# Optimization experiments

Hardware: AMD Instinct MI355X
Metric: run time of the kernel (lower is better)

## Reference

```python
import jax, jax.numpy as jnp
import numpy as np
from jax import lax

DROP_PROB = 0.1
BLOCK_SIZE = 7
FEAT_SIZE = 56
GAMMA = DROP_PROB / BLOCK_SIZE ** 2 * (FEAT_SIZE ** 2 / (FEAT_SIZE - BLOCK_SIZE + 1) ** 2)


def setup_inputs() -> dict:
    key = jax.random.key(0)
    k1, k2 = jax.random.split(key)
    x = jax.random.normal(k1, (32, 256, 56, 56), dtype=jnp.float32)
    u = jax.random.uniform(k2, (56, 56), dtype=jnp.float32)
    return {"x": x, "u": u}


def reference(x, u):
    # Bernoulli(gamma) seed mask over (H, W)
    mask = (u < GAMMA).astype(x.dtype)
    # Original code scatters 1s at seed + offsets in [0, block)^2 (down/right),
    # then crops to (H, W). Equivalent: backward-looking max window of size block.
    dilated = lax.reduce_window(
        mask, jnp.array(0.0, x.dtype), lax.max,
        window_dimensions=(BLOCK_SIZE, BLOCK_SIZE),
        window_strides=(1, 1),
        padding=((BLOCK_SIZE - 1, 0), (BLOCK_SIZE - 1, 0)),
    )
    block_mask = 1.0 - dilated  # (H, W), 0 inside dropped blocks
    scale = block_mask.size / jnp.sum(block_mask)
    return x * block_mask[None, None, :, :] * scale
```

## Files before the change

### kernel.cpp

```cpp
#include <hip/hip_runtime.h>


#define HW      3136
#define WDIM    56
#define HDIM    56
#define HW4     784
#define ROWMASK 0x00FFFFFFFFFFFFFFull
#define NBLOCKS 2009u
#define STRIDE  514304u
#define NVEC    6422528u
#define REM     250880u

typedef float vfloat4 __attribute__((ext_vector_type(4)));

__global__ void __launch_bounds__(256, 8) dropblock_fused_kernel(
        const float* __restrict__ u, const vfloat4* __restrict__ x,
        vfloat4* __restrict__ out) {
    __shared__ unsigned long long chunks[49];
    __shared__ unsigned long long dropbits[HDIM];
    __shared__ float s_scale;

    const float gamma = (float)(0.1 / 49.0 * (3136.0 / 2500.0));

    const unsigned int t = blockIdx.x * 256u + threadIdx.x;
    const int lane = threadIdx.x & 63;
    const int wave = threadIdx.x >> 6;

    float u0  = u[threadIdx.x];
    float u1  = u[threadIdx.x + 256];
    float u2  = u[threadIdx.x + 512];
    float u3  = u[threadIdx.x + 768];
    float u4  = u[threadIdx.x + 1024];
    float u5  = u[threadIdx.x + 1280];
    float u6  = u[threadIdx.x + 1536];
    float u7  = u[threadIdx.x + 1792];
    float u8  = u[threadIdx.x + 2048];
    float u9  = u[threadIdx.x + 2304];
    float u10 = u[threadIdx.x + 2560];
    float u11 = u[threadIdx.x + 2816];
    float ulast = 0.0f;
    if (wave == 0) ulast = u[3072 + lane];

    vfloat4 a0 = x[t];
    vfloat4 a1 = x[t + STRIDE];
    vfloat4 a2 = x[t + 2u * STRIDE];
    vfloat4 a3 = x[t + 3u * STRIDE];

    {
        unsigned long long b;
        b = __ballot(u0  < gamma); if (lane == 0) chunks[ 0 + wave] = b;
        b = __ballot(u1  < gamma); if (lane == 0) chunks[ 4 + wave] = b;
        b = __ballot(u2  < gamma); if (lane == 0) chunks[ 8 + wave] = b;
        b = __ballot(u3  < gamma); if (lane == 0) chunks[12 + wave] = b;
        b = __ballot(u4  < gamma); if (lane == 0) chunks[16 + wave] = b;
        b = __ballot(u5  < gamma); if (lane == 0) chunks[20 + wave] = b;
        b = __ballot(u6  < gamma); if (lane == 0) chunks[24 + wave] = b;
        b = __ballot(u7  < gamma); if (lane == 0) chunks[28 + wave] = b;
        b = __ballot(u8  < gamma); if (lane == 0) chunks[32 + wave] = b;
        b = __ballot(u9  < gamma); if (lane == 0) chunks[36 + wave] = b;
        b = __ballot(u10 < gamma); if (lane == 0) chunks[40 + wave] = b;
        b = __ballot(u11 < gamma); if (lane == 0) chunks[44 + wave] = b;
        if (wave == 0) {
            b = __ballot(ulast < gamma);
            if (lane == 0) chunks[48] = b;
        }
    }
    __syncthreads();

    if (wave == 0) {
        const int r = lane;
        unsigned long long rd = 0ull;
        if (r < HDIM) {
            int bit = r * WDIM;
            int a = bit >> 6, off = bit & 63;
            unsigned long long row = chunks[a] >> off;
            if (off > 8) row |= chunks[a + 1] << (64 - off);
            row &= ROWMASK;
            rd = row;
            #pragma unroll
            for (int k = 1; k < 7; ++k) rd |= row << k;
            rd &= ROWMASK;
        }
        unsigned long long d = rd;
        #pragma unroll
        for (int k = 1; k <= 6; ++k)
            d |= __shfl_up(rd, k);
        int kept = 0;
        if (r < HDIM) {
            dropbits[r] = d;
            kept = WDIM - __popcll(d);
        }
        #pragma unroll
        for (int s = 32; s; s >>= 1) kept += __shfl_xor(kept, s);
        if (lane == 0) s_scale = (float)HW / (float)kept;
    }
    __syncthreads();

    vfloat4 m;
    {
        const unsigned int q = t % (unsigned int)HW4;
        const int r = (int)q / 14;
        const int c0 = ((int)q - r * 14) * 4;
        const unsigned long long d = dropbits[r];
        const float scale = s_scale;
        m[0] = ((d >> c0) & 1ull) ? 0.0f : scale;
        m[1] = ((d >> (c0 + 1)) & 1ull) ? 0.0f : scale;
        m[2] = ((d >> (c0 + 2)) & 1ull) ? 0.0f : scale;
        m[3] = ((d >> (c0 + 3)) & 1ull) ? 0.0f : scale;
    }

    const bool ht = t < REM;

    vfloat4 b0 = x[t + 4u * STRIDE];
    vfloat4 b1 = x[t + 5u * STRIDE];
    vfloat4 b2 = x[t + 6u * STRIDE];
    vfloat4 b3 = x[t + 7u * STRIDE];
    __builtin_nontemporal_store(a0 * m, &out[t]);
    __builtin_nontemporal_store(a1 * m, &out[t + STRIDE]);
    __builtin_nontemporal_store(a2 * m, &out[t + 2u * STRIDE]);
    __builtin_nontemporal_store(a3 * m, &out[t + 3u * STRIDE]);
    vfloat4 c0 = x[t + 8u * STRIDE];
    vfloat4 c1 = x[t + 9u * STRIDE];
    vfloat4 c2 = x[t + 10u * STRIDE];
    vfloat4 c3 = x[t + 11u * STRIDE];
    vfloat4 d0;
    if (ht) d0 = x[t + 12u * STRIDE];
    __builtin_nontemporal_store(b0 * m, &out[t + 4u * STRIDE]);
    __builtin_nontemporal_store(b1 * m, &out[t + 5u * STRIDE]);
    __builtin_nontemporal_store(b2 * m, &out[t + 6u * STRIDE]);
    __builtin_nontemporal_store(b3 * m, &out[t + 7u * STRIDE]);
    __builtin_nontemporal_store(c0 * m, &out[t + 8u * STRIDE]);
    __builtin_nontemporal_store(c1 * m, &out[t + 9u * STRIDE]);
    __builtin_nontemporal_store(c2 * m, &out[t + 10u * STRIDE]);
    __builtin_nontemporal_store(c3 * m, &out[t + 11u * STRIDE]);
    if (ht) __builtin_nontemporal_store(d0 * m, &out[t + 12u * STRIDE]);
}

extern "C" void kernel_launch(void* const* d_in, const int* in_sizes, int n_in,
                              void* d_out, int out_size, void* d_ws, size_t ws_size,
                              hipStream_t stream) {
    const float* x = (const float*)d_in[0];
    const float* u = (const float*)d_in[1];
    float* out = (float*)d_out;

    dropblock_fused_kernel<<<NBLOCKS, 256, 0, stream>>>(
        u, (const vfloat4*)x, (vfloat4*)out);
}
```

Measured before the change: 184.8 us.

## Use more blocks with four vectors per thread and a sched barrier

Grid grows from 2009 to 6272 blocks, and each thread now handles 4 float4 vectors instead of about 12-13. This removes the tail predicate and the interleaved load/store batches. A sched_barrier pins the x loads ahead of the mask computation so they stay in flight during it. The cost is that every block repeats the 3136-element u load, the ballots, the mask build and two syncthreads, roughly three times as often in total, against better latency hiding and finer-grained scheduling.

```diff
diff --git a/kernel.cpp b/kernel.cpp
--- a/kernel.cpp
+++ b/kernel.cpp
@@ -6,10 +6,9 @@
 #define HDIM    56
 #define HW4     784
 #define ROWMASK 0x00FFFFFFFFFFFFFFull
-#define NBLOCKS 2009u
-#define STRIDE  514304u
+#define NB      6272u
+#define NT      1605632u
 #define NVEC    6422528u
-#define REM     250880u
 
 typedef float vfloat4 __attribute__((ext_vector_type(4)));
 
@@ -42,9 +41,10 @@
     if (wave == 0) ulast = u[3072 + lane];
 
     vfloat4 a0 = x[t];
-    vfloat4 a1 = x[t + STRIDE];
-    vfloat4 a2 = x[t + 2u * STRIDE];
-    vfloat4 a3 = x[t + 3u * STRIDE];
+    vfloat4 a1 = x[t + NT];
+    vfloat4 a2 = x[t + 2u * NT];
+    vfloat4 a3 = x[t + 3u * NT];
+    __builtin_amdgcn_sched_barrier(0);
 
     {
         unsigned long long b;
@@ -109,31 +109,10 @@
         m[3] = ((d >> (c0 + 3)) & 1ull) ? 0.0f : scale;
     }
 
-    const bool ht = t < REM;
-
-    vfloat4 b0 = x[t + 4u * STRIDE];
-    vfloat4 b1 = x[t + 5u * STRIDE];
-    vfloat4 b2 = x[t + 6u * STRIDE];
-    vfloat4 b3 = x[t + 7u * STRIDE];
     __builtin_nontemporal_store(a0 * m, &out[t]);
-    __builtin_nontemporal_store(a1 * m, &out[t + STRIDE]);
-    __builtin_nontemporal_store(a2 * m, &out[t + 2u * STRIDE]);
-    __builtin_nontemporal_store(a3 * m, &out[t + 3u * STRIDE]);
-    vfloat4 c0 = x[t + 8u * STRIDE];
-    vfloat4 c1 = x[t + 9u * STRIDE];
-    vfloat4 c2 = x[t + 10u * STRIDE];
-    vfloat4 c3 = x[t + 11u * STRIDE];
-    vfloat4 d0;
-    if (ht) d0 = x[t + 12u * STRIDE];
-    __builtin_nontemporal_store(b0 * m, &out[t + 4u * STRIDE]);
-    __builtin_nontemporal_store(b1 * m, &out[t + 5u * STRIDE]);
-    __builtin_nontemporal_store(b2 * m, &out[t + 6u * STRIDE]);
-    __builtin_nontemporal_store(b3 * m, &out[t + 7u * STRIDE]);
-    __builtin_nontemporal_store(c0 * m, &out[t + 8u * STRIDE]);
-    __builtin_nontemporal_store(c1 * m, &out[t + 9u * STRIDE]);
-    __builtin_nontemporal_store(c2 * m, &out[t + 10u * STRIDE]);
-    __builtin_nontemporal_store(c3 * m, &out[t + 11u * STRIDE]);
-    if (ht) __builtin_nontemporal_store(d0 * m, &out[t + 12u * STRIDE]);
+    __builtin_nontemporal_store(a1 * m, &out[t + NT]);
+    __builtin_nontemporal_store(a2 * m, &out[t + 2u * NT]);
+    __builtin_nontemporal_store(a3 * m, &out[t + 3u * NT]);
 }
 
 extern "C" void kernel_launch(void* const* d_in, const int* in_sizes, int n_in,
@@ -143,6 +122,6 @@
     const float* u = (const float*)d_in[1];
     float* out = (float*)d_out;
 
-    dropblock_fused_kernel<<<NBLOCKS, 256, 0, stream>>>(
+    dropblock_fused_kernel<<<NB, 256, 0, stream>>>(
         u, (const vfloat4*)x, (vfloat4*)out);
 }
```

Result: no change. 182.3 us (-1.3%).
